# Optimization experiments

Hardware: AMD Instinct MI355X
Metric: run time of the kernel (lower is better)

The kernel has to match this reference:

```python
import jax, jax.numpy as jnp
import numpy as np

B, N, C, H = 4, 1025, 768, 12
KEEP_RATIO = 0.25
BETA = 1.0


def setup_inputs() -> dict:
    key = jax.random.key(0)
    k1, k2, k3, k4, k5 = jax.random.split(key, 5)
    x = jax.random.normal(k1, (B, N, C), dtype=jnp.float32)
    ucb_count_score = jax.random.uniform(k2, (H, N), dtype=jnp.float32)
    W_qkv = jax.random.normal(k3, (C, 3 * C), dtype=jnp.float32) * 0.02
    W_proj = jax.random.normal(k4, (C, C), dtype=jnp.float32) * 0.02
    b_proj = jax.random.normal(k5, (C,), dtype=jnp.float32) * 0.02
    return {"x": x, "ucb_count_score": ucb_count_score, "W_qkv": W_qkv,
            "W_proj": W_proj, "b_proj": b_proj, "counter": 100, "ucb_enabled": 1}


def reference(x, ucb_count_score, W_qkv, W_proj, b_proj, counter, ucb_enabled):
    Bn, Nn, Cn = x.shape
    Dh = Cn // H
    scale = Dh ** -0.5
    # qkv projection (no bias, qkv_bias=False)
    qkv = (x @ W_qkv).reshape(Bn, Nn, 3, H, Dh)
    q = jnp.transpose(qkv[:, :, 0], (0, 2, 1, 3))  # [B,H,N,Dh]
    k = jnp.transpose(qkv[:, :, 1], (0, 2, 1, 3))
    v = jnp.transpose(qkv[:, :, 2], (0, 2, 1, 3))
    attn_probs = jax.nn.softmax(jnp.einsum('bhnd,bhmd->bhnm', q, k) * scale, axis=-1)

    if ucb_enabled and counter > 50:
        # UCB pruning path (exclude_cls=True, keep_ratio set)
        total_patches = Nn - 1
        k_sel = max(1, int(total_patches * KEEP_RATIO))
        patch_scores = attn_probs[:, :, :, 1:].mean(axis=2)  # [B,H,N-1]
        expl = BETA * jnp.sqrt(jnp.log(counter + 1.0) / (ucb_count_score[:, 1:] + 1e-6))  # [H,N-1]
        global_ucb = (patch_scores + expl[None]).mean(axis=1)  # [B,N-1]
        _, sel = jax.lax.top_k(global_ucb, k_sel)  # [B,k]
        tok = sel + 1  # shift for CLS
        # keep[b,j] = 1 if token j is CLS or selected in batch b
        keep = jnp.zeros((Bn, Nn), dtype=attn_probs.dtype)
        keep = keep.at[jnp.arange(Bn)[:, None], tok].set(1.0).at[:, 0].set(1.0)
        # mask[b,h,i,j] = keep[b,i] OR keep[b,j]
        mask = jnp.maximum(keep[:, None, :, None], keep[:, None, None, :])
        pruned = attn_probs * mask
        pruned = pruned / (pruned.sum(axis=-1, keepdims=True) + 1e-8)
        context = jnp.einsum('bhnm,bhmd->bhnd', pruned, v)
        cnt = jnp.zeros((Nn,), dtype=jnp.float32).at[tok.reshape(-1)].add(1.0) / Bn
        score_delta = jnp.broadcast_to(cnt[None, :], ucb_count_score.shape)
    else:
        context = jnp.einsum('bhnm,bhmd->bhnd', attn_probs, v)
        score_delta = None

    out = context.transpose(0, 2, 1, 3).reshape(Bn, Nn, Cn) @ W_proj + b_proj
    return out, score_delta
```

## Files before the change

### kernel.cpp

```cpp
#include <hip/hip_runtime.h>
#include <hip/hip_bf16.h>
#include <math.h>

#define Bb 4
#define Nn 1025
#define Cc 768
#define Hh 12
#define BH (Bb*Hh)
#define M_ROWS 4100
#define KSEL 256
#define JP 1152
#define IT_TILES 68
#define NIB32 33
#define NSW 9
#define MT16 264
#define KC24 24
#define JT16 72
#define JT32 36
#define STR4 292
#define NPART 396
#define NSCORE 1024
#define QSCALE 0.18033688011112042f
#define MBIAS -30000.0f

#define CAST_X_BLK 1584
#define CAST_WQKV_BLK 864
#define CAST_WPROJ_BLK 288

typedef __attribute__((ext_vector_type(8))) short short8;
typedef __attribute__((ext_vector_type(4))) float floatx4;
typedef __attribute__((ext_vector_type(4))) unsigned uintx4;

static __device__ inline unsigned short f2bf(float v) {
    __hip_bfloat16 b = __float2bfloat16(v);
    return *reinterpret_cast<unsigned short*>(&b);
}
static __device__ inline float fexp2(float x) {
    return __builtin_amdgcn_exp2f(x);
}
static __device__ inline unsigned pkbf(float lo, float hi) {
    union { float f; unsigned u; } a, b;
    a.f = lo; b.f = hi;
    return (a.u >> 16) | (b.u & 0xffff0000u);
}

static __device__ inline void async16(const unsigned short* g, unsigned short* l) {
    __builtin_amdgcn_global_load_lds(
        (const __attribute__((address_space(1))) unsigned int*)g,
        (__attribute__((address_space(3))) unsigned int*)l, 16, 0, 0);
}

__global__ __launch_bounds__(256)
void cast_all(const float* __restrict__ x, const float* __restrict__ Wqkv,
              const float* __restrict__ Wproj,
              unsigned short* __restrict__ xA, unsigned short* __restrict__ WB,
              unsigned short* __restrict__ WpB)
{
    int blk = blockIdx.x;
    int tid = threadIdx.x;
    if (blk < CAST_X_BLK) {
        int s = blk * 256 + tid;
        int ml = s & 15, q = (s >> 4) & 3;
        int t2 = s >> 6;
        int mt = t2 % MT16, kc = t2 / MT16;
        int m = mt * 16 + ml, k = kc * 32 + q * 8;
        uint4 pk = {0u, 0u, 0u, 0u};
        if (m < M_ROWS) {
            float4 a = *(const float4*)&x[(size_t)m * 768 + k];
            float4 b2 = *(const float4*)&x[(size_t)m * 768 + k + 4];
            pk.x = (unsigned)f2bf(a.x)  | ((unsigned)f2bf(a.y)  << 16);
            pk.y = (unsigned)f2bf(a.z)  | ((unsigned)f2bf(a.w)  << 16);
            pk.z = (unsigned)f2bf(b2.x) | ((unsigned)f2bf(b2.y) << 16);
            pk.w = (unsigned)f2bf(b2.z) | ((unsigned)f2bf(b2.w) << 16);
        }
        *(uint4*)&xA[(size_t)s * 8] = pk;
        return;
    }
    const float* W;
    unsigned short* WO;
    int N, NT, s;
    if (blk < CAST_X_BLK + CAST_WQKV_BLK) {
        W = Wqkv; WO = WB; N = 2304; NT = 144;
        s = (blk - CAST_X_BLK) * 256 + tid;
    } else {
        W = Wproj; WO = WpB; N = 768; NT = 48;
        s = (blk - CAST_X_BLK - CAST_WQKV_BLK) * 256 + tid;
    }
    int nl = s & 15, q = (s >> 4) & 3;
    int t2 = s >> 6;
    int nt = t2 % NT, kc = t2 / NT;
    int n = nt * 16 + nl, k = kc * 32 + q * 8;
    unsigned hv[8];
#pragma unroll
    for (int e = 0; e < 8; ++e)
        hv[e] = f2bf(W[(size_t)(k + e) * N + n]);
    uint4 pk;
    pk.x = hv[0] | (hv[1] << 16);
    pk.y = hv[2] | (hv[3] << 16);
    pk.z = hv[4] | (hv[5] << 16);
    pk.w = hv[6] | (hv[7] << 16);
    *(uint4*)&WO[(size_t)s * 8] = pk;
}

template<int NT, int MODE>
__global__ __launch_bounds__(256, 3)
void gemm_mfma(const unsigned short* __restrict__ Af,
               const unsigned short* __restrict__ Bf,
               int Nt16,
               unsigned short* __restrict__ qB, unsigned short* __restrict__ kF,
               unsigned short* __restrict__ vF,
               float* __restrict__ outp, const float* __restrict__ bias)
{
    __shared__ __align__(16) unsigned short ldsA[4096];
    __shared__ __align__(16) unsigned short ldsB[NT * 1024];
    const int tid = threadIdx.x;
    const int ln = tid & 63, w = tid >> 6;
    const int wm = w >> 1, wn = w & 1;
    const int mb = blockIdx.x, nb = blockIdx.y;

    floatx4 acc[4][NT];
#pragma unroll
    for (int mt = 0; mt < 4; ++mt)
#pragma unroll
        for (int nt = 0; nt < NT; ++nt)
            acc[mt][nt] = (floatx4){0.f, 0.f, 0.f, 0.f};

    for (int kc = 0; kc < KC24; ++kc) {
        const unsigned short* gA = Af + ((size_t)(kc * MT16 + mb * 8)) * 512;
        const unsigned short* gB = Bf + ((size_t)(kc * Nt16 + nb * (NT * 2))) * 512;
        async16(gA + (size_t)(w * 128 + ln) * 8,      &ldsA[w * 1024]);
        async16(gA + (size_t)(w * 128 + 64 + ln) * 8, &ldsA[w * 1024 + 512]);
        if (NT == 4) {
            async16(gB + (size_t)(w * 128 + ln) * 8,      &ldsB[w * 1024]);
            async16(gB + (size_t)(w * 128 + 64 + ln) * 8, &ldsB[w * 1024 + 512]);
        } else {
            async16(gB + (size_t)(w * 64 + ln) * 8, &ldsB[w * 512]);
        }
        __syncthreads();

        short8 Am[4], Bn[NT];
#pragma unroll
        for (int mt = 0; mt < 4; ++mt)
            Am[mt] = *(const short8*)&ldsA[((wm * 4 + mt) * 64 + ln) * 8];
#pragma unroll
        for (int nt = 0; nt < NT; ++nt)
            Bn[nt] = *(const short8*)&ldsB[((wn * NT + nt) * 64 + ln) * 8];
#pragma unroll
        for (int mt = 0; mt < 4; ++mt)
#pragma unroll
            for (int nt = 0; nt < NT; ++nt)
                acc[mt][nt] = __builtin_amdgcn_mfma_f32_16x16x32_bf16(
                    Am[mt], Bn[nt], acc[mt][nt], 0, 0, 0);
        __syncthreads();
    }

    const int q = ln >> 4, l15 = ln & 15;
    if (MODE == 1) {
#pragma unroll
        for (int nt = 0; nt < NT; ++nt) {
            int gn = nb * (NT * 32) + wn * (NT * 16) + nt * 16 + l15;
            float bv = bias[gn];
#pragma unroll
            for (int mt = 0; mt < 4; ++mt) {
                int gmb = mb * 128 + wm * 64 + mt * 16 + q * 4;
#pragma unroll
                for (int r = 0; r < 4; ++r) {
                    int gm = gmb + r;
                    if (gm < M_ROWS)
                        outp[(size_t)gm * 768 + gn] = acc[mt][nt][r] + bv;
                }
            }
        }
    } else {
#pragma unroll
        for (int nt = 0; nt < NT; ++nt) {
            int gn = nb * (NT * 32) + wn * (NT * 16) + nt * 16 + l15;
            int s = (gn >= 1536) ? 2 : (gn >= 768 ? 1 : 0);
            int rr = gn - s * Cc;
            int h = rr >> 6, d = rr & 63;
#pragma unroll
            for (int mt = 0; mt < 4; ++mt) {
                int gmb = mb * 128 + wm * 64 + mt * 16 + q * 4;
#pragma unroll
                for (int r = 0; r < 4; ++r) {
                    int gm = gmb + r;
                    if (gm >= M_ROWS) continue;
                    int b = gm / Nn;
                    int n = gm - b * Nn;
                    int bh = b * Hh + h;
                    float val = acc[mt][nt][r];
                    if (s == 0) {
                        int idx = (((bh * IT_TILES + (n >> 4)) * 2 + (d >> 5)) * 512)
                                  + ((((d & 31) >> 3) * 16 + (n & 15)) * 8) + (d & 7);
                        qB[idx] = f2bf(val * QSCALE);
                    } else if (s == 1) {
                        size_t idx = ((((size_t)bh * JT16 + (n >> 4)) * 2 + (d >> 5)) * 64
                                      + ((d >> 3) & 3) * 16 + (n & 15)) * 8 + (d & 7);
                        kF[idx] = f2bf(val);
                    } else {
                        size_t idx = ((((size_t)bh * JT32 + (n >> 5)) * 4 + (d >> 4)) * 64
                                      + ((n >> 3) & 3) * 16 + (d & 15)) * 8 + (n & 7);
                        vF[idx] = f2bf(val);
                    }
                }
            }
        }
    }
}

__global__ __launch_bounds__(256, 4)
void attn_colsum_mfma(const unsigned short* __restrict__ qB,
                      const unsigned short* __restrict__ kF,
                      float* __restrict__ colsum_part)
{
    __shared__ unsigned int expS8[32 * STR4];
    __shared__ float red16[16][32];
    __shared__ float linv[32];

    const int blk = blockIdx.x;
    const int x8 = blk & 7, g = blk >> 3;
    const int bh = x8 * 6 + (g % 6);
    const int ib = g / 6;
    const int tid = threadIdx.x;
    const int ws = tid >> 6;
    const int ln = tid & 63;
    const int i16 = ln & 15, q = ln >> 4;

    const unsigned short* kBase = kF + (size_t)bh * JT16 * 1024;

    short8 Qf[2][2];
#pragma unroll
    for (int it = 0; it < 2; ++it)
#pragma unroll
        for (int kc = 0; kc < 2; ++kc)
            Qf[it][kc] = *(const short8*)&qB[(((size_t)bh * IT_TILES + ib * 2 + it) * 2 + kc) * 512 + ln * 8];

    float lacc[2][2] = {{0.f, 0.f}, {0.f, 0.f}};

    short8 Kc[2][2], Kn[2][2];
#pragma unroll
    for (int jt = 0; jt < 2; ++jt)
#pragma unroll
        for (int kc = 0; kc < 2; ++kc)
            Kc[jt][kc] = *(const short8*)&kBase[(((ws * 2 + jt) * 2 + kc) * 64 + ln) * 8];

    for (int sw = 0; sw < NSW; ++sw) {
        if (sw + 1 < NSW) {
#pragma unroll
            for (int jt = 0; jt < 2; ++jt)
#pragma unroll
                for (int kc = 0; kc < 2; ++kc)
                    Kn[jt][kc] = *(const short8*)&kBase[((((sw + 1) * 8 + ws * 2 + jt) * 2 + kc) * 64 + ln) * 8];
        }

        floatx4 S[2][2];
#pragma unroll
        for (int it = 0; it < 2; ++it)
#pragma unroll
            for (int jt = 0; jt < 2; ++jt) {
                S[it][jt] = (floatx4){0.f, 0.f, 0.f, 0.f};
#pragma unroll
                for (int kc = 0; kc < 2; ++kc)
                    S[it][jt] = __builtin_amdgcn_mfma_f32_16x16x32_bf16(Kc[jt][kc], Qf[it][kc], S[it][jt], 0, 0, 0);
            }

        const int jbase0 = sw * 128 + ws * 32 + q * 4;
#pragma unroll
        for (int it = 0; it < 2; ++it) {
            const int irow = it * 16 + i16;
#pragma unroll
            for (int jt = 0; jt < 2; ++jt) {
                int jbase = jbase0 + jt * 16;
                float p[4];
                if (sw < NSW - 1) {
#pragma unroll
                    for (int r = 0; r < 4; ++r)
                        p[r] = fexp2(S[it][jt][r]);
                } else {
#pragma unroll
                    for (int r = 0; r < 4; ++r) {
                        float vld = (jbase + r < Nn) ? 1.f : 0.f;
                        p[r] = fexp2(S[it][jt][r]) * vld;
                    }
                }
                lacc[it][jt] += (p[0] + p[1]) + (p[2] + p[3]);
                unsigned u = (unsigned)__builtin_amdgcn_cvt_pk_fp8_f32(p[0], p[1], 0, false);
                u = (unsigned)__builtin_amdgcn_cvt_pk_fp8_f32(p[2], p[3], (int)u, true);
                expS8[irow * STR4 + (jbase >> 2)] = u;
            }
        }
#pragma unroll
        for (int jt = 0; jt < 2; ++jt)
#pragma unroll
            for (int kc = 0; kc < 2; ++kc)
                Kc[jt][kc] = Kn[jt][kc];
    }

    __syncthreads();
#pragma unroll
    for (int it = 0; it < 2; ++it)
        red16[ws * 4 + q][it * 16 + i16] = lacc[it][0] + lacc[it][1];
    __syncthreads();
    if (tid < 32) {
        float s = 0.f;
#pragma unroll
        for (int t = 0; t < 16; ++t) s += red16[t][tid];
        int gi = ib * 32 + tid;
        linv[tid] = (gi < Nn) ? 1.f / s : 0.f;
    }
    __syncthreads();

    float* prow = colsum_part + (size_t)(bh * NIB32 + ib) * JP;
    for (int grp = tid; grp < 288; grp += 256) {
        float a0 = 0.f, a1 = 0.f, a2 = 0.f, a3 = 0.f;
#pragma unroll 8
        for (int i = 0; i < 32; ++i) {
            unsigned v = expS8[i * STR4 + grp];
            float li = linv[i];
            a0 += __builtin_amdgcn_cvt_f32_fp8(v, 0) * li;
            a1 += __builtin_amdgcn_cvt_f32_fp8(v, 1) * li;
            a2 += __builtin_amdgcn_cvt_f32_fp8(v, 2) * li;
            a3 += __builtin_amdgcn_cvt_f32_fp8(v, 3) * li;
        }
        float4 o = {a0, a1, a2, a3};
        *(float4*)&prow[grp * 4] = o;
    }
}

__global__ __launch_bounds__(256)
void colsum_reduce(const float* __restrict__ colsum_part,
                   const float* __restrict__ ucb_score,
                   const int* __restrict__ counter_p,
                   float* __restrict__ scoreF)
{
    const int b = blockIdx.x, jc = blockIdx.y;
    const int tid = threadIdx.x;
    const int j32 = tid & 31, grp = tid >> 5;
    const int t = jc * 32 + j32 + 1;
    __shared__ float red[8][32];

    const float* pb = colsum_part + (size_t)b * NPART * JP + t;
    float a0 = 0.f, a1 = 0.f;
    int r = grp;
    for (; r + 8 < NPART; r += 16) {
        a0 += pb[(size_t)r * JP];
        a1 += pb[(size_t)(r + 8) * JP];
    }
    for (; r < NPART; r += 8) a0 += pb[(size_t)r * JP];
    red[grp][j32] = a0 + a1;
    __syncthreads();

    if (tid < 32) {
        float cs = 0.f;
#pragma unroll
        for (int g = 0; g < 8; ++g) cs += red[g][tid];
        int tt = jc * 32 + tid + 1;
        float lc = logf((float)(*counter_p) + 1.0f);
        float s = cs * (1.0f / (float)Nn);
#pragma unroll
        for (int h = 0; h < Hh; ++h)
            s += sqrtf(lc / (ucb_score[h * Nn + tt] + 1e-6f));
        s *= (1.0f / (float)Hh);
        scoreF[b * NSCORE + tt - 1] = s;
    }
}

__global__ __launch_bounds__(1024)
void ucb_topk(const float* __restrict__ scoreF,
              float* __restrict__ keepP, float* __restrict__ cnt_b)
{
    const int b = blockIdx.x;
    const int tid = threadIdx.x;
    const int w = tid >> 6, ln = tid & 63;
    __shared__ int hist[8192];
    __shared__ int wtot[16];
    __shared__ unsigned ckey[1024];
    __shared__ int cidx[1024];
    __shared__ int s_tb, s_rem, ccount;

    for (int tpos = tid; tpos < JP; tpos += 1024) {
        keepP[b * JP + tpos] = 0.f;
        cnt_b[b * JP + tpos] = 0.f;
    }

    const unsigned key = __float_as_uint(scoreF[b * NSCORE + tid]);

    for (int tpos = tid; tpos < 8192; tpos += 1024) hist[tpos] = 0;
    if (tid == 0) ccount = 0;
    __syncthreads();
    atomicAdd(&hist[key >> 18], 1);
    __syncthreads();

    int part = 0;
#pragma unroll
    for (int q2 = 0; q2 < 8; ++q2) part += hist[tid * 8 + q2];
    int v = part;
#pragma unroll
    for (int off = 1; off < 64; off <<= 1) {
        int tv = __shfl_down(v, off);
        if (ln + off < 64) v += tv;
    }
    if (ln == 0) wtot[w] = v;
    __syncthreads();
    int woff = 0;
    for (int w2 = w + 1; w2 < 16; ++w2) woff += wtot[w2];
    int cum_above = v + woff - part;
    for (int q2 = 7; q2 >= 0; --q2) {
        int c = hist[tid * 8 + q2];
        if (cum_above < KSEL && cum_above + c >= KSEL) {
            s_tb = tid * 8 + q2;
            s_rem = KSEL - cum_above;
        }
        cum_above += c;
    }
    __syncthreads();

    const int tb = s_tb, rem = s_rem;
    const int mybin = (int)(key >> 18);
    bool sel = mybin > tb;
    if (mybin == tb) {
        int p = atomicAdd(&ccount, 1);
        ckey[p] = key; cidx[p] = tid;
    }
    __syncthreads();
    if (mybin == tb) {
        int rr = 0;
        const int cc = ccount;
        for (int c = 0; c < cc; ++c) {
            unsigned kc2 = ckey[c]; int ic = cidx[c];
            if (kc2 > key || (kc2 == key && ic < tid)) ++rr;
        }
        sel = rr < rem;
    }
    if (sel) {
        int tok = tid + 1;
        keepP[b * JP + tok] = 1.f;
        cnt_b[b * JP + tok] = 1.0f / (float)Bb;
    }
    if (tid == 0) keepP[b * JP + 0] = 1.f;
}

__global__ __launch_bounds__(256, 2)
void attn_ctx_mfma(const unsigned short* __restrict__ qB,
                   const unsigned short* __restrict__ kF,
                   const unsigned short* __restrict__ vF,
                   const float* __restrict__ keepP, const float* __restrict__ cnt_b,
                   unsigned short* __restrict__ ctxA, float* __restrict__ out2)
{
    __shared__ float keeps[JP];
    __shared__ float red16s[4][64];
    __shared__ float redC[64][66];

    const int blk = blockIdx.x;
    const int x8 = blk & 7, g = blk >> 3;
    const int bh = x8 * 6 + (g % 6);
    const int ib = g / 6;
    const int b = bh / Hh, h = bh % Hh;
    const int tid = threadIdx.x;
    const int ws = tid >> 6;
    const int ln = tid & 63;
    const int i16 = ln & 15, q = ln >> 4;

    {
        int t = blk * 256 + tid;
        if (t < Hh * Nn) {
            int n = t % Nn;
            out2[t] = cnt_b[0 * JP + n] + cnt_b[1 * JP + n]
                    + cnt_b[2 * JP + n] + cnt_b[3 * JP + n];
        }
    }

    for (int t = tid; t < JP; t += 256) keeps[t] = keepP[b * JP + t];

    const unsigned short* kBase = kF + (size_t)bh * JT16 * 1024;
    const unsigned short* vBase = vF + (size_t)bh * JT32 * 2048;

    short8 Qf[4][2];
#pragma unroll
    for (int it = 0; it < 4; ++it)
#pragma unroll
        for (int kc = 0; kc < 2; ++kc)
            Qf[it][kc] = *(const short8*)&qB[(((size_t)bh * IT_TILES + ib * 4 + it) * 2 + kc) * 512 + ln * 8];

    __syncthreads();

    float keepi[4];
#pragma unroll
    for (int it = 0; it < 4; ++it)
        keepi[it] = keeps[(ib * 4 + it) * 16 + i16];

    floatx4 ctxacc[4][4];
#pragma unroll
    for (int it = 0; it < 4; ++it)
#pragma unroll
        for (int dt = 0; dt < 4; ++dt)
            ctxacc[it][dt] = (floatx4){0.f, 0.f, 0.f, 0.f};
    floatx4 ds4[4];
#pragma unroll
    for (int it = 0; it < 4; ++it) ds4[it] = (floatx4){0.f, 0.f, 0.f, 0.f};

    const short obf = (short)0x3F80;
    const short8 onesB = {obf, obf, obf, obf, obf, obf, obf, obf};

    short8 Kc[2][2], Kn[2][2];
    short8 Vc8[4], Vn8[4];
#pragma unroll
    for (int jt = 0; jt < 2; ++jt)
#pragma unroll
        for (int kc = 0; kc < 2; ++kc)
            Kc[jt][kc] = *(const short8*)&kBase[(((ws * 2 + jt) * 2 + kc) * 64 + ln) * 8];
#pragma unroll
    for (int dt = 0; dt < 4; ++dt)
        Vc8[dt] = *(const short8*)&vBase[(((size_t)ws * 4 + dt) * 64 + ln) * 8];

    for (int sw = 0; sw < NSW; ++sw) {
        if (sw + 1 < NSW) {
#pragma unroll
            for (int jt = 0; jt < 2; ++jt)
#pragma unroll
                for (int kc = 0; kc < 2; ++kc)
                    Kn[jt][kc] = *(const short8*)&kBase[((((sw + 1) * 8 + ws * 2 + jt) * 2 + kc) * 64 + ln) * 8];
#pragma unroll
            for (int dt = 0; dt < 4; ++dt)
                Vn8[dt] = *(const short8*)&vBase[((((size_t)(sw + 1) * 4 + ws) * 4 + dt) * 64 + ln) * 8];
        }

        float biasK[2][4], biasN[2][4];
#pragma unroll
        for (int jt = 0; jt < 2; ++jt)
#pragma unroll
            for (int r = 0; r < 4; ++r) {
                int jj = sw * 128 + ws * 32 + jt * 16 + q * 4 + r;
                biasK[jt][r] = (jj < Nn) ? 0.f : MBIAS;
                biasN[jt][r] = (keeps[jj] - 1.f) * 30000.f;
            }

#pragma unroll
        for (int it = 0; it < 4; ++it) {
            bool rk = keepi[it] > 0.5f;
            floatx4 S[2];
#pragma unroll
            for (int jt = 0; jt < 2; ++jt)
#pragma unroll
                for (int r = 0; r < 4; ++r)
                    S[jt][r] = rk ? biasK[jt][r] : biasN[jt][r];
#pragma unroll
            for (int jt = 0; jt < 2; ++jt)
#pragma unroll
                for (int kc = 0; kc < 2; ++kc)
                    S[jt] = __builtin_amdgcn_mfma_f32_16x16x32_bf16(Kc[jt][kc], Qf[it][kc], S[jt], 0, 0, 0);

            float p0[4], p1[4];
#pragma unroll
            for (int r = 0; r < 4; ++r) {
                p0[r] = fexp2(S[0][r]);
                p1[r] = fexp2(S[1][r]);
            }
            unsigned Au = pkbf(p0[0], p0[1]);
            unsigned Bu = pkbf(p0[2], p0[3]);
            unsigned Cu = pkbf(p1[0], p1[1]);
            unsigned Du = pkbf(p1[2], p1[3]);
            asm("v_permlane32_swap_b32 %0, %1" : "+v"(Au), "+v"(Cu));
            asm("v_permlane32_swap_b32 %0, %1" : "+v"(Bu), "+v"(Du));
            asm("v_permlane16_swap_b32 %0, %1" : "+v"(Au), "+v"(Cu));
            asm("v_permlane16_swap_b32 %0, %1" : "+v"(Bu), "+v"(Du));
            short8 Wf = __builtin_bit_cast(short8, (uintx4){Au, Bu, Cu, Du});
#pragma unroll
            for (int dt = 0; dt < 4; ++dt)
                ctxacc[it][dt] = __builtin_amdgcn_mfma_f32_16x16x32_bf16(
                    Wf, Vc8[dt], ctxacc[it][dt], 0, 0, 0);
            ds4[it] = __builtin_amdgcn_mfma_f32_16x16x32_bf16(
                Wf, onesB, ds4[it], 0, 0, 0);
        }

#pragma unroll
        for (int jt = 0; jt < 2; ++jt)
#pragma unroll
            for (int kc = 0; kc < 2; ++kc)
                Kc[jt][kc] = Kn[jt][kc];
#pragma unroll
        for (int dt = 0; dt < 4; ++dt)
            Vc8[dt] = Vn8[dt];
    }

    __syncthreads();
    if (i16 == 0) {
#pragma unroll
        for (int it = 0; it < 4; ++it)
#pragma unroll
            for (int r = 0; r < 4; ++r)
                red16s[ws][it * 16 + q * 4 + r] = ds4[it][r];
    }
    for (int w = 0; w < 4; ++w) {
        __syncthreads();
        if (ws == w) {
#pragma unroll
            for (int it = 0; it < 4; ++it)
#pragma unroll
                for (int dt = 0; dt < 4; ++dt)
#pragma unroll
                    for (int r = 0; r < 4; ++r) {
                        int i = it * 16 + q * 4 + r;
                        int d = dt * 16 + i16;
                        float v = ctxacc[it][dt][r];
                        redC[i][d] = (w == 0) ? v : (redC[i][d] + v);
                    }
        }
    }
    __syncthreads();
#pragma unroll
    for (int rep = 0; rep < 2; ++rep) {
        int s2 = tid + rep * 256;
        int i = s2 >> 3, dc = s2 & 7;
        int gi = ib * 64 + i;
        if (gi < Nn) {
            int m = b * Nn + gi;
            float den = red16s[0][i] + red16s[1][i] + red16s[2][i] + red16s[3][i];
            float dv = 1.f / (den + 1e-8f);
            const float* src = &redC[i][dc * 8];
            uint4 pk;
            pk.x = (unsigned)f2bf(src[0] * dv) | ((unsigned)f2bf(src[1] * dv) << 16);
            pk.y = (unsigned)f2bf(src[2] * dv) | ((unsigned)f2bf(src[3] * dv) << 16);
            pk.z = (unsigned)f2bf(src[4] * dv) | ((unsigned)f2bf(src[5] * dv) << 16);
            pk.w = (unsigned)f2bf(src[6] * dv) | ((unsigned)f2bf(src[7] * dv) << 16);
            int kc2 = h * 2 + (dc >> 2);
            int q2 = dc & 3;
            size_t idx = (((size_t)(kc2 * MT16 + (m >> 4))) * 64 + q2 * 16 + (m & 15)) * 8;
            *(uint4*)&ctxA[idx] = pk;
        }
    }
}

extern "C" void kernel_launch(void* const* d_in, const int* in_sizes, int n_in,
                              void* d_out, int out_size, void* d_ws, size_t ws_size,
                              hipStream_t stream) {
    const float* x     = (const float*)d_in[0];
    const float* ucb   = (const float*)d_in[1];
    const float* Wqkv  = (const float*)d_in[2];
    const float* Wproj = (const float*)d_in[3];
    const float* bproj = (const float*)d_in[4];
    const int*   counter = (const int*)d_in[5];

    unsigned short* qB = (unsigned short*)d_ws;
    unsigned short* kF = qB + 3342336;
    unsigned short* vF = kF + 3538944;
    float* keepP    = (float*)(vF + 3538944);
    float* cnt_b    = keepP + 4608;
    unsigned short* ctxA = (unsigned short*)(cnt_b + 4608);
    unsigned short* xA   = ctxA + 3244032;
    unsigned short* WB   = xA + 3244032;
    unsigned short* WpB  = WB + 1769472;
    float* colsum_part = (float*)(WpB + 589824);
    float* scoreF = colsum_part + 1824768;

    float* out  = (float*)d_out;
    float* out2 = out + 3148800;

    cast_all<<<dim3(CAST_X_BLK + CAST_WQKV_BLK + CAST_WPROJ_BLK), dim3(256), 0, stream>>>(
        x, Wqkv, Wproj, xA, WB, WpB);
    gemm_mfma<4, 0><<<dim3(33, 18), dim3(256), 0, stream>>>(
        xA, WB, 144, qB, kF, vF, nullptr, nullptr);
    attn_colsum_mfma<<<dim3(8 * 198), dim3(256), 0, stream>>>(qB, kF, colsum_part);
    colsum_reduce<<<dim3(Bb, 32), dim3(256), 0, stream>>>(colsum_part, ucb, counter, scoreF);
    ucb_topk<<<dim3(Bb), dim3(1024), 0, stream>>>(scoreF, keepP, cnt_b);
    attn_ctx_mfma<<<dim3(8 * 102), dim3(256), 0, stream>>>(qB, kF, vF, keepP, cnt_b, ctxA, out2);
    gemm_mfma<2, 1><<<dim3(33, 12), dim3(256), 0, stream>>>(
        ctxA, WpB, 48, nullptr, nullptr, nullptr, out, bproj);
}
```

Baseline: 200.5 us.

## Raise attention kernel occupancy by dropping prefetch and MFMA row-sum

Raises the launch-bounds occupancy hint for the attention-context kernel from 2 to 3 blocks per CU. To cut register pressure it removes the double-buffered K/V register prefetch and loads each tile inside the loop. It also replaces the extra MFMA against a ones vector for the softmax denominator with scalar fp32 partial sums reduced through shared memory. This trades explicit load/compute overlap for more resident waves, and the denominator is now summed from fp32 rather than bf16-rounded probabilities.

Measured after the change: 214.0 us. +6.7%, slower.

```diff
diff --git a/kernel.cpp b/kernel.cpp
--- a/kernel.cpp
+++ b/kernel.cpp
@@ -440,7 +440,7 @@
     if (tid == 0) keepP[b * JP + 0] = 1.f;
 }
 
-__global__ __launch_bounds__(256, 2)
+__global__ __launch_bounds__(256, 3)
 void attn_ctx_mfma(const unsigned short* __restrict__ qB,
                    const unsigned short* __restrict__ kF,
                    const unsigned short* __restrict__ vF,
@@ -448,7 +448,8 @@
                    unsigned short* __restrict__ ctxA, float* __restrict__ out2)
 {
     __shared__ float keeps[JP];
-    __shared__ float red16s[4][64];
+    __shared__ float red16[16][64];
+    __shared__ float dinv[64];
     __shared__ float redC[64][66];
 
     const int blk = blockIdx.x;
@@ -495,35 +496,18 @@
 #pragma unroll
         for (int dt = 0; dt < 4; ++dt)
             ctxacc[it][dt] = (floatx4){0.f, 0.f, 0.f, 0.f};
-    floatx4 ds4[4];
-#pragma unroll
-    for (int it = 0; it < 4; ++it) ds4[it] = (floatx4){0.f, 0.f, 0.f, 0.f};
-
-    const short obf = (short)0x3F80;
-    const short8 onesB = {obf, obf, obf, obf, obf, obf, obf, obf};
-
-    short8 Kc[2][2], Kn[2][2];
-    short8 Vc8[4], Vn8[4];
-#pragma unroll
-    for (int jt = 0; jt < 2; ++jt)
-#pragma unroll
-        for (int kc = 0; kc < 2; ++kc)
-            Kc[jt][kc] = *(const short8*)&kBase[(((ws * 2 + jt) * 2 + kc) * 64 + ln) * 8];
-#pragma unroll
-    for (int dt = 0; dt < 4; ++dt)
-        Vc8[dt] = *(const short8*)&vBase[(((size_t)ws * 4 + dt) * 64 + ln) * 8];
+    float dsacc[4] = {0.f, 0.f, 0.f, 0.f};
 
     for (int sw = 0; sw < NSW; ++sw) {
-        if (sw + 1 < NSW) {
-#pragma unroll
-            for (int jt = 0; jt < 2; ++jt)
-#pragma unroll
-                for (int kc = 0; kc < 2; ++kc)
-                    Kn[jt][kc] = *(const short8*)&kBase[((((sw + 1) * 8 + ws * 2 + jt) * 2 + kc) * 64 + ln) * 8];
-#pragma unroll
-            for (int dt = 0; dt < 4; ++dt)
-                Vn8[dt] = *(const short8*)&vBase[((((size_t)(sw + 1) * 4 + ws) * 4 + dt) * 64 + ln) * 8];
-        }
+        short8 Kc[2][2], Vc8[4];
+#pragma unroll
+        for (int jt = 0; jt < 2; ++jt)
+#pragma unroll
+            for (int kc = 0; kc < 2; ++kc)
+                Kc[jt][kc] = *(const short8*)&kBase[(((size_t)(sw * 8 + ws * 2 + jt) * 2 + kc) * 64 + ln) * 8];
+#pragma unroll
+        for (int dt = 0; dt < 4; ++dt)
+            Vc8[dt] = *(const short8*)&vBase[((((size_t)sw * 4 + ws) * 4 + dt) * 64 + ln) * 8];
 
         float biasK[2][4], biasN[2][4];
 #pragma unroll
@@ -556,6 +540,8 @@
                 p0[r] = fexp2(S[0][r]);
                 p1[r] = fexp2(S[1][r]);
             }
+            dsacc[it] += ((p0[0] + p0[1]) + (p0[2] + p0[3]))
+                       + ((p1[0] + p1[1]) + (p1[2] + p1[3]));
             unsigned Au = pkbf(p0[0], p0[1]);
             unsigned Bu = pkbf(p0[2], p0[3]);
             unsigned Cu = pkbf(p1[0], p1[1]);
@@ -569,27 +555,18 @@
             for (int dt = 0; dt < 4; ++dt)
                 ctxacc[it][dt] = __builtin_amdgcn_mfma_f32_16x16x32_bf16(
                     Wf, Vc8[dt], ctxacc[it][dt], 0, 0, 0);
-            ds4[it] = __builtin_amdgcn_mfma_f32_16x16x32_bf16(
-                Wf, onesB, ds4[it], 0, 0, 0);
-        }
-
-#pragma unroll
-        for (int jt = 0; jt < 2; ++jt)
-#pragma unroll
-            for (int kc = 0; kc < 2; ++kc)
-                Kc[jt][kc] = Kn[jt][kc];
-#pragma unroll
-        for (int dt = 0; dt < 4; ++dt)
-            Vc8[dt] = Vn8[dt];
-    }
-
-    __syncthreads();
-    if (i16 == 0) {
-#pragma unroll
-        for (int it = 0; it < 4; ++it)
-#pragma unroll
-            for (int r = 0; r < 4; ++r)
-                red16s[ws][it * 16 + q * 4 + r] = ds4[it][r];
+        }
+    }
+
+    __syncthreads();
+#pragma unroll
+    for (int it = 0; it < 4; ++it) red16[ws * 4 + q][it * 16 + i16] = dsacc[it];
+    __syncthreads();
+    if (tid < 64) {
+        float s = 0.f;
+#pragma unroll
+        for (int t = 0; t < 16; ++t) s += red16[t][tid];
+        dinv[tid] = 1.f / (s + 1e-8f);
     }
     for (int w = 0; w < 4; ++w) {
         __syncthreads();
@@ -615,8 +592,7 @@
         int gi = ib * 64 + i;
         if (gi < Nn) {
             int m = b * Nn + gi;
-            float den = red16s[0][i] + red16s[1][i] + red16s[2][i] + red16s[3][i];
-            float dv = 1.f / (den + 1e-8f);
+            float dv = dinv[i];
             const float* src = &redC[i][dc * 8];
             uint4 pk;
             pk.x = (unsigned)f2bf(src[0] * dv) | ((unsigned)f2bf(src[1] * dv) << 16);
```
